# Optimization experiments

Hardware: AMD Instinct MI355X
Metric: run time of the kernel (lower is better)

The kernel has to match this reference:

```python
import jax, jax.numpy as jnp
import numpy as np

V, T, H, N, HID = 512, 64, 256, 1024, 100
D = V + T  # biLSTM input dim


def _lstm_dir(x, Wih, Whh, b, reverse):
    # x: [n, Din]; PyTorch gate order i,f,g,o; b = b_ih + b_hh (equivalent math)
    xw = x @ Wih.T + b  # [n, 4H] precomputed input projection
    if reverse:
        xw = xw[::-1]
    h_dim = Whh.shape[1]

    def step(carry, xt):
        h, c = carry
        g = xt + h @ Whh.T
        i, f, gg, o = jnp.split(g, 4, axis=-1)
        i = jax.nn.sigmoid(i)
        f = jax.nn.sigmoid(f)
        gg = jnp.tanh(gg)
        o = jax.nn.sigmoid(o)
        c = f * c + i * gg
        h = o * jnp.tanh(c)
        return (h, c), h

    init = (jnp.zeros((h_dim,), x.dtype), jnp.zeros((h_dim,), x.dtype))
    _, hs = jax.lax.scan(step, init, xw)
    return hs[::-1] if reverse else hs


def setup_inputs() -> dict:
    key = jax.random.key(0)
    ks = jax.random.split(key, 20)
    s = 1.0 / np.sqrt(H)  # PyTorch LSTM init scale
    inp = {
        "word_table": jax.random.normal(ks[0], (V, V), jnp.float32) * 0.1,
        "pos_table": jax.random.normal(ks[1], (T, T), jnp.float32) * 0.1,
        # layer 0 fwd/bwd
        "l0f_Wih": jax.random.uniform(ks[2], (4 * H, D), jnp.float32, -s, s),
        "l0f_Whh": jax.random.uniform(ks[3], (4 * H, H), jnp.float32, -s, s),
        "l0f_b": jax.random.uniform(ks[4], (4 * H,), jnp.float32, -s, s),
        "l0b_Wih": jax.random.uniform(ks[5], (4 * H, D), jnp.float32, -s, s),
        "l0b_Whh": jax.random.uniform(ks[6], (4 * H, H), jnp.float32, -s, s),
        "l0b_b": jax.random.uniform(ks[7], (4 * H,), jnp.float32, -s, s),
        # layer 1 fwd/bwd (input = 2H)
        "l1f_Wih": jax.random.uniform(ks[8], (4 * H, 2 * H), jnp.float32, -s, s),
        "l1f_Whh": jax.random.uniform(ks[9], (4 * H, H), jnp.float32, -s, s),
        "l1f_b": jax.random.uniform(ks[10], (4 * H,), jnp.float32, -s, s),
        "l1b_Wih": jax.random.uniform(ks[11], (4 * H, 2 * H), jnp.float32, -s, s),
        "l1b_Whh": jax.random.uniform(ks[12], (4 * H, H), jnp.float32, -s, s),
        "l1b_b": jax.random.uniform(ks[13], (4 * H,), jnp.float32, -s, s),
        # edge-scorer MLP: Linear(4H,100) -> tanh -> Linear(100,1)
        "mlp_W1": jax.random.uniform(ks[14], (HID, 4 * H), jnp.float32, -0.03, 0.03),
        "mlp_b1": jax.random.uniform(ks[15], (HID,), jnp.float32, -0.03, 0.03),
        "mlp_W2": jax.random.uniform(ks[16], (1, HID), jnp.float32, -0.1, 0.1),
        "mlp_b2": jax.random.uniform(ks[17], (1,), jnp.float32, -0.1, 0.1),
        "word_idx": jax.random.randint(ks[18], (1, N), 0, V),
        "pos_idx": jax.random.randint(ks[19], (1, N), 0, T),
    }
    return inp


def reference(word_table, pos_table,
              l0f_Wih, l0f_Whh, l0f_b, l0b_Wih, l0b_Whh, l0b_b,
              l1f_Wih, l1f_Whh, l1f_b, l1b_Wih, l1b_Whh, l1b_b,
              mlp_W1, mlp_b1, mlp_W2, mlp_b2,
              word_idx, pos_idx):
    # embedding lookups on external tables, cat word+pos -> [n, D]
    x = jnp.concatenate([word_table[word_idx[0]], pos_table[pos_idx[0]]], axis=-1)
    # 2-layer bidirectional LSTM, batch=1 (squeezed)
    h = jnp.concatenate([_lstm_dir(x, l0f_Wih, l0f_Whh, l0f_b, False),
                         _lstm_dir(x, l0b_Wih, l0b_Whh, l0b_b, True)], axis=-1)  # [n, 2H]
    h = jnp.concatenate([_lstm_dir(h, l1f_Wih, l1f_Whh, l1f_b, False),
                         _lstm_dir(h, l1b_Wih, l1b_Whh, l1b_b, True)], axis=-1)  # [n, 2H]
    # pairwise edge scorer: layer_2(tanh(layer_1(cat(h_head, h_mod))))
    # split W1 = [Wh | Wm] so the cat never materializes per pair
    two_h = h.shape[-1]
    Wh, Wm = mlp_W1[:, :two_h], mlp_W1[:, two_h:]
    A = h @ Wh.T  # [n, HID] head contribution
    B = h @ Wm.T  # [n, HID] modifier contribution
    hid = jnp.tanh(A[:, None, :] + B[None, :, :] + mlp_b1)  # [n, n, HID]
    scores = hid @ mlp_W2[0] + mlp_b2[0]  # [n, n]
    n = scores.shape[0]
    eye = jnp.eye(n, dtype=bool)
    scores = jnp.where(eye, 0.0, scores)  # diagonal left at 0, as in the torch loop
    return jax.nn.softmax(scores, axis=0)
```

## Files before the change

### kernel.cpp

```cpp
#include <hip/hip_runtime.h>
#include <hip/hip_bf16.h>


#define L2E 1.4426950408889634f

__device__ __forceinline__ float fast_rcp(float x) { return __builtin_amdgcn_rcpf(x); }
__device__ __forceinline__ float sigm_f(float x) {
    return fast_rcp(1.f + exp2f(-x * L2E));
}
__device__ __forceinline__ float tanh_f(float x) {
    return 1.f - 2.f * fast_rcp(1.f + exp2f(x * (2.f * L2E)));
}

__device__ __forceinline__ void st_msg(unsigned long long* p, unsigned long long m) {
    asm volatile("global_store_dwordx2 %0, %1, off sc0 sc1"
                 :: "v"(p), "v"(m) : "memory");
}

__device__ __forceinline__ unsigned long long poll_msg(
    const unsigned long long* p, unsigned want)
{
    unsigned long long r0, r1, r2, r3, r = 0;
    bool done = false;
    for (int it = 0; it < 8192 && !done; ++it) {
        asm volatile(
            "global_load_dwordx2 %0, %4, off sc0 sc1\n\t"
            "global_load_dwordx2 %1, %4, off sc0 sc1\n\t"
            "global_load_dwordx2 %2, %4, off sc0 sc1\n\t"
            "global_load_dwordx2 %3, %4, off sc0 sc1\n\t"
            "s_waitcnt vmcnt(3)"
            : "=&v"(r0), "=&v"(r1), "=&v"(r2), "=&v"(r3)
            : "v"(p) : "memory");
        if (__all((unsigned)(r0 >> 32) == want)) { r = r0; done = true; }
        if (!done) {
            asm volatile("s_waitcnt vmcnt(2)" ::: "memory");
            if (__all((unsigned)(r1 >> 32) == want)) { r = r1; done = true; }
        }
        if (!done) {
            asm volatile("s_waitcnt vmcnt(1)" ::: "memory");
            if (__all((unsigned)(r2 >> 32) == want)) { r = r2; done = true; }
        }
        if (!done) {
            asm volatile("s_waitcnt vmcnt(0)" ::: "memory");
            if (__all((unsigned)(r3 >> 32) == want)) { r = r3; done = true; }
        }
        asm volatile("s_waitcnt vmcnt(0)" ::: "memory");
    }
    if (!done) {
        do {
            r = __hip_atomic_load(p, __ATOMIC_RELAXED, __HIP_MEMORY_SCOPE_AGENT);
        } while (!__all((unsigned)(r >> 32) == want));
    }
    return r;
}

__global__ __launch_bounds__(256) void embed_kernel(
    const float* __restrict__ wt, const float* __restrict__ pt,
    const int* __restrict__ wi, const int* __restrict__ pi,
    float* __restrict__ x)
{
    int idx = blockIdx.x * 256 + threadIdx.x;
    if (idx >= 1024 * 576) return;
    int n = idx / 576, c = idx % 576;
    x[idx] = (c < 512) ? wt[wi[n] * 512 + c] : pt[pi[n] * 64 + (c - 512)];
}

__global__ __launch_bounds__(256) void gemm_bias(
    const float* __restrict__ A,
    const float* __restrict__ W0, const float* __restrict__ W1,
    const float* __restrict__ b0, const float* __restrict__ b1,
    float* __restrict__ C0, float* __restrict__ C1,
    int M, int N, int K)
{
    const float* W = blockIdx.z ? W1 : W0;
    const float* bias = blockIdx.z ? b1 : b0;
    float* C = blockIdx.z ? C1 : C0;
    int m0 = blockIdx.y * 64, n0 = blockIdx.x * 64;
    __shared__ float As[16][65];
    __shared__ float Ws[16][65];
    int tid = threadIdx.x;
    int tx = tid & 15, ty = tid >> 4;
    float acc[4][4] = {};
    int lr = tid >> 2, lkc = (tid & 3) * 4;
    for (int k0 = 0; k0 < K; k0 += 16) {
        float4 a4 = *(const float4*)&A[(size_t)(m0 + lr) * K + k0 + lkc];
        float4 w4 = *(const float4*)&W[(size_t)(n0 + lr) * K + k0 + lkc];
        As[lkc + 0][lr] = a4.x; As[lkc + 1][lr] = a4.y;
        As[lkc + 2][lr] = a4.z; As[lkc + 3][lr] = a4.w;
        Ws[lkc + 0][lr] = w4.x; Ws[lkc + 1][lr] = w4.y;
        Ws[lkc + 2][lr] = w4.z; Ws[lkc + 3][lr] = w4.w;
        __syncthreads();
#pragma unroll
        for (int k = 0; k < 16; k++) {
            float a[4], b[4];
#pragma unroll
            for (int i = 0; i < 4; i++) a[i] = As[k][ty * 4 + i];
#pragma unroll
            for (int j = 0; j < 4; j++) b[j] = Ws[k][tx * 4 + j];
#pragma unroll
            for (int i = 0; i < 4; i++)
#pragma unroll
                for (int j = 0; j < 4; j++) acc[i][j] += a[i] * b[j];
        }
        __syncthreads();
    }
    int colbase = n0 + tx * 4;
    float4 bv = *(const float4*)&bias[colbase];
#pragma unroll
    for (int i = 0; i < 4; i++) {
        float4 o;
        o.x = acc[i][0] + bv.x; o.y = acc[i][1] + bv.y;
        o.z = acc[i][2] + bv.z; o.w = acc[i][3] + bv.w;
        *(float4*)&C[(size_t)(m0 + ty * 4 + i) * N + colbase] = o;
    }
}

__global__ __launch_bounds__(512, 2) void lstm_scan(
    const float* __restrict__ xw_f, const float* __restrict__ xw_b,
    const float* __restrict__ Whh_f, const float* __restrict__ Whh_b,
    float* __restrict__ hout,
    unsigned long long* __restrict__ hx)
{
    const int sub  = blockIdx.x;
    const int tid  = threadIdx.x;
    const int lane = tid & 63;
    const int wv   = tid >> 6;
    const int dsel = tid >> 8;
    const int tl   = tid & 255;
    const int kh   = tl >> 7;
    const int lrow = tl & 127;
    const int gi   = lrow >> 5;
    const int R    = gi * 256 + sub * 32 + (lrow & 31);

    const float* __restrict__ xw  = dsel ? xw_b : xw_f;
    const float* __restrict__ Whh = dsel ? Whh_b : Whh_f;

    float4 w4[16];
    {
        const float4* Wr = (const float4*)(Whh + (size_t)R * 256 + (kh << 7));
#pragma unroll
        for (int i = 0; i < 16; i++) w4[i] = Wr[i];
    }

    __shared__ float h0_sh[256], h1_sh[256];
    __shared__ float part0[256], part1[256];
    __shared__ float gact0[128], gact1[128];
    float* __restrict__ h_sh  = dsel ? h1_sh : h0_sh;
    float* __restrict__ partd = dsel ? part1 : part0;
    float* __restrict__ gactd = dsel ? gact1 : gact0;

    float c = 0.f;
    float xwv = 0.f;
    if (tl < 128) xwv = xw[(size_t)(dsel ? 1023 : 0) * 1024 + R];
    if (tid < 256) { h0_sh[tid] = 0.f; h1_sh[tid] = 0.f; }
    __syncthreads();

    for (int t = 0; t < 1024; t++) {
        float a0 = 0.f, a1 = 0.f, a2 = 0.f, a3 = 0.f;
        const float4* hp4 = (const float4*)&h_sh[kh << 7];
#pragma unroll
        for (int i = 0; i < 16; i += 4) {
            float4 h0v = hp4[i + 0], w0v = w4[i + 0];
            float4 h1v = hp4[i + 1], w1v = w4[i + 1];
            float4 h2v = hp4[i + 2], w2v = w4[i + 2];
            float4 h3v = hp4[i + 3], w3v = w4[i + 3];
            a0 += w0v.x * h0v.x + w0v.y * h0v.y + w0v.z * h0v.z + w0v.w * h0v.w;
            a1 += w1v.x * h1v.x + w1v.y * h1v.y + w1v.z * h1v.z + w1v.w * h1v.w;
            a2 += w2v.x * h2v.x + w2v.y * h2v.y + w2v.z * h2v.z + w2v.w * h2v.w;
            a3 += w3v.x * h3v.x + w3v.y * h3v.y + w3v.z * h3v.z + w3v.w * h3v.w;
        }
        partd[tl] = (a0 + a1) + (a2 + a3);
        __syncthreads();

        if (tl < 128) {
            float s = partd[tl] + partd[128 + tl] + xwv;
            gactd[tl] = (gi == 2) ? tanh_f(s) : sigm_f(s);
            if (t + 1 < 1024) {
                int trown = dsel ? (1022 - t) : (t + 1);
                xwv = xw[(size_t)trown * 1024 + R];
            }
        }
        __syncthreads();

        const int par = (t + 1) & 1;
        if (wv == 0 || wv == 4) {
            if (lane < 32) {
                float iv = gactd[lane], fv = gactd[32 + lane],
                      gv = gactd[64 + lane], ov = gactd[96 + lane];
                c = fv * c + iv * gv;
                float h = ov * tanh_f(c);
                if (t + 1 < 1024) {
                    unsigned long long msg =
                        ((unsigned long long)(unsigned)(t + 1) << 32) |
                        (unsigned long long)__float_as_uint(h);
                    st_msg(&hx[(((sub << 1) + par) << 6) + (dsel << 5) + lane], msg);
                    h_sh[sub * 32 + lane] = h;
                }
                int trow = dsel ? (1023 - t) : t;
                hout[(size_t)trow * 512 + (dsel << 8) + sub * 32 + lane] = h;
            }
        }
        if (wv != 0 && t + 1 < 1024) {
            int pw = (sub + wv) & 7;
            const unsigned long long* sp =
                &hx[(((pw << 1) + par) << 6) + lane];
            unsigned long long v = poll_msg(sp, (unsigned)(t + 1));
            float hv = __uint_as_float((unsigned)v);
            ((lane < 32) ? h0_sh : h1_sh)[pw * 32 + (lane & 31)] = hv;
        }
        __syncthreads();

#pragma unroll
        for (int i = 0; i < 16; i++)
            asm volatile("" : "+v"(w4[i].x), "+v"(w4[i].y),
                              "+v"(w4[i].z), "+v"(w4[i].w));
    }
}

__global__ __launch_bounds__(256) void transpose_w1(
    const float* __restrict__ W1, float* __restrict__ W1T)
{
    int idx = blockIdx.x * 256 + threadIdx.x;
    if (idx >= 100 * 1024) return;
    int n = idx / 1024, j = idx % 1024;
    W1T[j * 100 + n] = W1[idx];
}

__global__ __launch_bounds__(256) void ab_kernel(
    const float* __restrict__ h1, const float* __restrict__ W1T,
    const float* __restrict__ b1v,
    float* __restrict__ Ab, float* __restrict__ Bb)
{
    int m0 = blockIdx.x * 16;
    __shared__ float hs[16][512];
    int tid = threadIdx.x;
    for (int idx = tid * 4; idx < 16 * 512; idx += 1024) {
        int r = idx >> 9, cc = idx & 511;
        *(float4*)&hs[r][cc] = *(const float4*)&h1[(size_t)(m0 + r) * 512 + cc];
    }
    __syncthreads();
    bool isB = tid >= 128;
    int n = tid & 127;
    if (n < 100) {
        float acc[16] = {};
        const float* wbase = W1T + (isB ? 512 * 100 : 0) + n;
#pragma unroll 4
        for (int k = 0; k < 512; k++) {
            float wv = wbase[k * 100];
#pragma unroll
            for (int m = 0; m < 16; m++) acc[m] += hs[m][k] * wv;
        }
        float badd = isB ? 0.f : b1v[n];
        float* dst = isB ? Bb : Ab;
#pragma unroll
        for (int m = 0; m < 16; m++) dst[(m0 + m) * 100 + n] = acc[m] + badd;
    }
}

__global__ __launch_bounds__(256) void pair_kernel(
    const float* __restrict__ Ab, const float* __restrict__ Bb,
    const float* __restrict__ W2, const float* __restrict__ b2,
    float* __restrict__ sT)
{
    int i0 = blockIdx.x * 32, j0 = blockIdx.y * 32;
    __shared__ float Ash[32][101];
    __shared__ float Bsh[32][101];
    __shared__ float w2s[100];
    int tid = threadIdx.x;
    for (int idx = tid; idx < 3200; idx += 256) {
        int r = idx / 100, cc = idx % 100;
        Ash[r][cc] = Ab[(i0 + r) * 100 + cc];
        Bsh[r][cc] = Bb[(j0 + r) * 100 + cc];
    }
    if (tid < 100) w2s[tid] = W2[tid];
    __syncthreads();
    float b2v = b2[0];
    int il = (tid & 15) * 2, jl = (tid >> 4) * 2;
    float a00 = 0.f, a01 = 0.f, a10 = 0.f, a11 = 0.f;
#pragma unroll 4
    for (int k = 0; k < 100; k++) {
        float wv = w2s[k];
        float x0 = Ash[il][k], x1 = Ash[il + 1][k];
        float y0 = Bsh[jl][k], y1 = Bsh[jl + 1][k];
        a00 += wv * tanh_f(x0 + y0);
        a01 += wv * tanh_f(x0 + y1);
        a10 += wv * tanh_f(x1 + y0);
        a11 += wv * tanh_f(x1 + y1);
    }
    float vals[2][2] = {{a00, a01}, {a10, a11}};
#pragma unroll
    for (int a = 0; a < 2; a++)
#pragma unroll
        for (int b = 0; b < 2; b++) {
            int gi2 = i0 + il + a, gj = j0 + jl + b;
            float v = vals[a][b] + b2v;
            if (gi2 == gj) v = 0.f;
            sT[(size_t)gj * 1024 + gi2] = v;
        }
}

__global__ __launch_bounds__(256) void colstats(
    const float* __restrict__ sT, float* __restrict__ mx, float* __restrict__ rs)
{
    int j = blockIdx.x;
    const float* row = sT + (size_t)j * 1024;
    int tid = threadIdx.x;
    __shared__ float red[256];
    float m = -INFINITY;
    for (int i = tid; i < 1024; i += 256) m = fmaxf(m, row[i]);
    red[tid] = m; __syncthreads();
    for (int s = 128; s > 0; s >>= 1) {
        if (tid < s) red[tid] = fmaxf(red[tid], red[tid + s]);
        __syncthreads();
    }
    float mxv = red[0];
    __syncthreads();
    float ssum = 0.f;
    for (int i = tid; i < 1024; i += 256) ssum += exp2f((row[i] - mxv) * L2E);
    red[tid] = ssum; __syncthreads();
    for (int s = 128; s > 0; s >>= 1) {
        if (tid < s) red[tid] += red[tid + s];
        __syncthreads();
    }
    if (tid == 0) { mx[j] = mxv; rs[j] = 1.f / red[0]; }
}

__global__ __launch_bounds__(256) void writeout(
    const float* __restrict__ sT, const float* __restrict__ mx,
    const float* __restrict__ rs, float* __restrict__ out)
{
    int i0 = blockIdx.x * 32, j0 = blockIdx.y * 32;
    __shared__ float til[32][33];
    int tid = threadIdx.x;
    int r = tid >> 3, c4 = (tid & 7) * 4;
    float4 v = *(const float4*)&sT[(size_t)(j0 + r) * 1024 + i0 + c4];
    til[r][c4 + 0] = v.x; til[r][c4 + 1] = v.y;
    til[r][c4 + 2] = v.z; til[r][c4 + 3] = v.w;
    __syncthreads();
    float4 o;
    float* op = &out[(size_t)(i0 + r) * 1024 + j0 + c4];
    o.x = exp2f((til[c4 + 0][r] - mx[j0 + c4 + 0]) * L2E) * rs[j0 + c4 + 0];
    o.y = exp2f((til[c4 + 1][r] - mx[j0 + c4 + 1]) * L2E) * rs[j0 + c4 + 1];
    o.z = exp2f((til[c4 + 2][r] - mx[j0 + c4 + 2]) * L2E) * rs[j0 + c4 + 2];
    o.w = exp2f((til[c4 + 3][r] - mx[j0 + c4 + 3]) * L2E) * rs[j0 + c4 + 3];
    *(float4*)op = o;
}

extern "C" void kernel_launch(void* const* d_in, const int* in_sizes, int n_in,
                              void* d_out, int out_size, void* d_ws, size_t ws_size,
                              hipStream_t stream)
{
    const float* word_table = (const float*)d_in[0];
    const float* pos_table  = (const float*)d_in[1];
    const float* l0f_Wih = (const float*)d_in[2];
    const float* l0f_Whh = (const float*)d_in[3];
    const float* l0f_b   = (const float*)d_in[4];
    const float* l0b_Wih = (const float*)d_in[5];
    const float* l0b_Whh = (const float*)d_in[6];
    const float* l0b_b   = (const float*)d_in[7];
    const float* l1f_Wih = (const float*)d_in[8];
    const float* l1f_Whh = (const float*)d_in[9];
    const float* l1f_b   = (const float*)d_in[10];
    const float* l1b_Wih = (const float*)d_in[11];
    const float* l1b_Whh = (const float*)d_in[12];
    const float* l1b_b   = (const float*)d_in[13];
    const float* mlp_W1  = (const float*)d_in[14];
    const float* mlp_b1  = (const float*)d_in[15];
    const float* mlp_W2  = (const float*)d_in[16];
    const float* mlp_b2  = (const float*)d_in[17];
    const int*   word_idx = (const int*)d_in[18];
    const int*   pos_idx  = (const int*)d_in[19];
    float* out = (float*)d_out;

    float* ws = (float*)d_ws;
    const size_t OFF_X   = 0;
    const size_t OFF_XWF = 589824;
    const size_t OFF_XWB = 1638400;
    const size_t OFF_H0  = 2686976;
    const size_t OFF_H1  = 3211264;
    const size_t OFF_W1T = 3735552;
    const size_t OFF_A   = 3837952;
    const size_t OFF_B   = 3940352;
    const size_t OFF_ST  = 4042752;
    const size_t OFF_MX  = 5091328;
    const size_t OFF_RS  = 5092352;
    const size_t OFF_HX  = 5095424;

    float* x   = ws + OFF_X;
    float* xwf = ws + OFF_XWF;
    float* xwb = ws + OFF_XWB;
    float* h0  = ws + OFF_H0;
    float* h1  = ws + OFF_H1;
    float* w1t = ws + OFF_W1T;
    float* Ab  = ws + OFF_A;
    float* Bb  = ws + OFF_B;
    float* sT  = ws + OFF_ST;
    float* mx  = ws + OFF_MX;
    float* rs  = ws + OFF_RS;
    unsigned long long* hx0 = (unsigned long long*)(ws + OFF_HX);
    unsigned long long* hx1 = hx0 + 1024;

    hipMemsetAsync(hx0, 0, 2048 * sizeof(unsigned long long), stream);

    embed_kernel<<<(1024 * 576 + 255) / 256, 256, 0, stream>>>(
        word_table, pos_table, word_idx, pos_idx, x);

    transpose_w1<<<(100 * 1024 + 255) / 256, 256, 0, stream>>>(mlp_W1, w1t);

    gemm_bias<<<dim3(16, 16, 2), 256, 0, stream>>>(
        x, l0f_Wih, l0b_Wih, l0f_b, l0b_b, xwf, xwb, 1024, 1024, 576);

    lstm_scan<<<8, 512, 0, stream>>>(
        xwf, xwb, l0f_Whh, l0b_Whh, h0, hx0);

    gemm_bias<<<dim3(16, 16, 2), 256, 0, stream>>>(
        h0, l1f_Wih, l1b_Wih, l1f_b, l1b_b, xwf, xwb, 1024, 1024, 512);

    lstm_scan<<<8, 512, 0, stream>>>(
        xwf, xwb, l1f_Whh, l1b_Whh, h1, hx1);

    ab_kernel<<<64, 256, 0, stream>>>(h1, w1t, mlp_b1, Ab, Bb);

    pair_kernel<<<dim3(32, 32), 256, 0, stream>>>(Ab, Bb, mlp_W2, mlp_b2, sT);

    colstats<<<1024, 256, 0, stream>>>(sT, mx, rs);

    writeout<<<dim3(32, 32), 256, 0, stream>>>(sT, mx, rs, out);
}
```

Before: 4.087 ms.

## Fuse gate activation into producer lanes and stream Whh from memory each step

Drops one __syncthreads per timestep: the 32 producer lanes per direction now compute all four gate activations themselves from the partial sums, so the shared gact buffer goes away. The Whh slice is no longer pinned in registers and is re-read from global memory every step. The xw input row is fetched at the start of each step instead of being prefetched. The poll loop gains s_sleep between loads and its iteration cap is halved. This trims a barrier and register pressure, but adds 512 bytes of per-thread weight traffic on every step of a latency-bound recurrence and puts the activation math on fewer lanes.

```diff
diff --git a/kernel.cpp b/kernel.cpp
--- a/kernel.cpp
+++ b/kernel.cpp
@@ -22,11 +22,14 @@
 {
     unsigned long long r0, r1, r2, r3, r = 0;
     bool done = false;
-    for (int it = 0; it < 8192 && !done; ++it) {
+    for (int it = 0; it < 4096 && !done; ++it) {
         asm volatile(
             "global_load_dwordx2 %0, %4, off sc0 sc1\n\t"
+            "s_sleep 3\n\t"
             "global_load_dwordx2 %1, %4, off sc0 sc1\n\t"
+            "s_sleep 3\n\t"
             "global_load_dwordx2 %2, %4, off sc0 sc1\n\t"
+            "s_sleep 3\n\t"
             "global_load_dwordx2 %3, %4, off sc0 sc1\n\t"
             "s_waitcnt vmcnt(3)"
             : "=&v"(r0), "=&v"(r1), "=&v"(r2), "=&v"(r3)
@@ -129,41 +132,41 @@
     const int tl   = tid & 255;
     const int kh   = tl >> 7;
     const int lrow = tl & 127;
-    const int gi   = lrow >> 5;
-    const int R    = gi * 256 + sub * 32 + (lrow & 31);
+    const int R    = (lrow >> 5) * 256 + sub * 32 + (lrow & 31);
 
     const float* __restrict__ xw  = dsel ? xw_b : xw_f;
     const float* __restrict__ Whh = dsel ? Whh_b : Whh_f;
-
-    float4 w4[16];
-    {
-        const float4* Wr = (const float4*)(Whh + (size_t)R * 256 + (kh << 7));
-#pragma unroll
-        for (int i = 0; i < 16; i++) w4[i] = Wr[i];
-    }
+    const float4* __restrict__ Wr =
+        (const float4*)(Whh + (size_t)R * 256 + (kh << 7));
 
     __shared__ float h0_sh[256], h1_sh[256];
     __shared__ float part0[256], part1[256];
-    __shared__ float gact0[128], gact1[128];
     float* __restrict__ h_sh  = dsel ? h1_sh : h0_sh;
     float* __restrict__ partd = dsel ? part1 : part0;
-    float* __restrict__ gactd = dsel ? gact1 : gact0;
-
+
+    const bool isProd = (wv == 0 || wv == 4) && lane < 32;
     float c = 0.f;
-    float xwv = 0.f;
-    if (tl < 128) xwv = xw[(size_t)(dsel ? 1023 : 0) * 1024 + R];
     if (tid < 256) { h0_sh[tid] = 0.f; h1_sh[tid] = 0.f; }
     __syncthreads();
 
     for (int t = 0; t < 1024; t++) {
+        const int trow = dsel ? (1023 - t) : t;
+
+        float xg0 = 0.f, xg1 = 0.f, xg2 = 0.f, xg3 = 0.f;
+        if (isProd) {
+            const float* xr = &xw[(size_t)trow * 1024 + sub * 32 + lane];
+            xg0 = xr[0];   xg1 = xr[256];
+            xg2 = xr[512]; xg3 = xr[768];
+        }
+
         float a0 = 0.f, a1 = 0.f, a2 = 0.f, a3 = 0.f;
         const float4* hp4 = (const float4*)&h_sh[kh << 7];
 #pragma unroll
         for (int i = 0; i < 16; i += 4) {
-            float4 h0v = hp4[i + 0], w0v = w4[i + 0];
-            float4 h1v = hp4[i + 1], w1v = w4[i + 1];
-            float4 h2v = hp4[i + 2], w2v = w4[i + 2];
-            float4 h3v = hp4[i + 3], w3v = w4[i + 3];
+            float4 h0v = hp4[i + 0], w0v = Wr[i + 0];
+            float4 h1v = hp4[i + 1], w1v = Wr[i + 1];
+            float4 h2v = hp4[i + 2], w2v = Wr[i + 2];
+            float4 h3v = hp4[i + 3], w3v = Wr[i + 3];
             a0 += w0v.x * h0v.x + w0v.y * h0v.y + w0v.z * h0v.z + w0v.w * h0v.w;
             a1 += w1v.x * h1v.x + w1v.y * h1v.y + w1v.z * h1v.z + w1v.w * h1v.w;
             a2 += w2v.x * h2v.x + w2v.y * h2v.y + w2v.z * h2v.z + w2v.w * h2v.w;
@@ -172,33 +175,24 @@
         partd[tl] = (a0 + a1) + (a2 + a3);
         __syncthreads();
 
-        if (tl < 128) {
-            float s = partd[tl] + partd[128 + tl] + xwv;
-            gactd[tl] = (gi == 2) ? tanh_f(s) : sigm_f(s);
+        const int par = (t + 1) & 1;
+        if (isProd) {
+            float s0 = partd[lane]      + partd[128 + lane]  + xg0;
+            float s1 = partd[32 + lane] + partd[160 + lane]  + xg1;
+            float s2 = partd[64 + lane] + partd[192 + lane]  + xg2;
+            float s3 = partd[96 + lane] + partd[224 + lane]  + xg3;
+            float iv = sigm_f(s0), fv = sigm_f(s1);
+            float gv = tanh_f(s2), ov = sigm_f(s3);
+            c = fv * c + iv * gv;
+            float h = ov * tanh_f(c);
             if (t + 1 < 1024) {
-                int trown = dsel ? (1022 - t) : (t + 1);
-                xwv = xw[(size_t)trown * 1024 + R];
+                unsigned long long msg =
+                    ((unsigned long long)(unsigned)(t + 1) << 32) |
+                    (unsigned long long)__float_as_uint(h);
+                st_msg(&hx[(((sub << 1) + par) << 6) + (dsel << 5) + lane], msg);
+                h_sh[sub * 32 + lane] = h;
             }
-        }
-        __syncthreads();
-
-        const int par = (t + 1) & 1;
-        if (wv == 0 || wv == 4) {
-            if (lane < 32) {
-                float iv = gactd[lane], fv = gactd[32 + lane],
-                      gv = gactd[64 + lane], ov = gactd[96 + lane];
-                c = fv * c + iv * gv;
-                float h = ov * tanh_f(c);
-                if (t + 1 < 1024) {
-                    unsigned long long msg =
-                        ((unsigned long long)(unsigned)(t + 1) << 32) |
-                        (unsigned long long)__float_as_uint(h);
-                    st_msg(&hx[(((sub << 1) + par) << 6) + (dsel << 5) + lane], msg);
-                    h_sh[sub * 32 + lane] = h;
-                }
-                int trow = dsel ? (1023 - t) : t;
-                hout[(size_t)trow * 512 + (dsel << 8) + sub * 32 + lane] = h;
-            }
+            hout[(size_t)trow * 512 + (dsel << 8) + sub * 32 + lane] = h;
         }
         if (wv != 0 && t + 1 < 1024) {
             int pw = (sub + wv) & 7;
@@ -209,11 +203,6 @@
             ((lane < 32) ? h0_sh : h1_sh)[pw * 32 + (lane & 31)] = hv;
         }
         __syncthreads();
-
-#pragma unroll
-        for (int i = 0; i < 16; i++)
-            asm volatile("" : "+v"(w4[i].x), "+v"(w4[i].y),
-                              "+v"(w4[i].z), "+v"(w4[i].w));
     }
 }
 
```

Result: no change. 4.097 ms (+0.2%).
